# Kernel optimization log

Hardware: AMD Instinct MI355X
Metric: run time of the kernel (lower is better)

## Reference

```python
import jax, jax.numpy as jnp
import numpy as np

B, L, S, H, E = 4, 2048, 2048, 8, 64


def setup_inputs() -> dict:
    key = jax.random.key(0)
    kq, kk, kv, kt = jax.random.split(key, 4)
    queries = jax.random.normal(kq, (B, L, H, E), dtype=jnp.float32)
    keys = jax.random.normal(kk, (B, S, H, E), dtype=jnp.float32)
    values = jax.random.normal(kv, (B, S, H, E), dtype=jnp.float32)
    # de-stationarization log-scale factor, kept small so exp(tau) ~ O(1)
    tau = 0.1 * jax.random.normal(kt, (B, 1, 1, 1), dtype=jnp.float32)
    # causal mask: True above the diagonal (positions to be masked)
    attn_mask = jnp.triu(jnp.ones((L, S), dtype=bool), k=1)
    return {"queries": queries, "keys": keys, "values": values,
            "attn_mask": attn_mask, "tau": tau}


def reference(queries, keys, values, attn_mask, tau):
    # queries: [B,L,H,E], keys/values: [B,S,H,E], tau: [B,1,1,1], mask: [L,S]
    E_ = queries.shape[-1]
    scale = 1.0 / jnp.sqrt(jnp.asarray(E_, dtype=queries.dtype))
    # scores: [B,H,L,S], with tau-based de-stationarization rescale
    scores = jnp.einsum('blhe,bshe->bhls', queries, keys) * (scale * jnp.exp(tau))
    scores = jnp.where(attn_mask, -jnp.inf, scores)
    A = jax.nn.softmax(scores, axis=-1)  # dropout is identity at inference
    V = jnp.einsum('bhls,bshd->blhd', A, values)
    return V
```

## Files before the change

### kernel.cpp

```cpp
#include <hip/hip_runtime.h>
#include <hip/hip_bf16.h>
#include <math.h>

#define B_ 4
#define L_ 2048
#define H_ 8
#define E_ 64
#define HE 512

typedef short bf16x8 __attribute__((ext_vector_type(8)));
typedef float f32x4 __attribute__((ext_vector_type(4)));
typedef float f32x16 __attribute__((ext_vector_type(16)));
typedef unsigned short u16x4 __attribute__((ext_vector_type(4)));
typedef unsigned short u16x8 __attribute__((ext_vector_type(8)));

__device__ __forceinline__ unsigned short f2b(float f) {
  return __builtin_bit_cast(unsigned short, (__hip_bfloat16)f);
}
__device__ __forceinline__ unsigned cvtpk(float lo, float hi) {
  unsigned r;
  asm("v_cvt_pk_bf16_f32 %0, %1, %2" : "=v"(r) : "v"(lo), "v"(hi));
  return r;
}
__device__ __forceinline__ void pl32swap(unsigned &a, unsigned &b) {
  asm volatile("v_permlane32_swap_b32 %0, %1" : "+v"(a), "+v"(b));
}

__global__ __launch_bounds__(512, 1) void attn_fwd(
    const float* __restrict__ Q, const float* __restrict__ K,
    const float* __restrict__ V, const float* __restrict__ tau,
    float* __restrict__ O)
{
  const int f  = blockIdx.x + 16 * (blockIdx.y + 8 * blockIdx.z);
  const int u  = f >> 5, hb = f & 31;
  const int h  = hb & 7, b = hb >> 3;
  const int qt = (u < 8) ? u : 23 - u;

  const int tid  = threadIdx.x;
  const int wave = tid >> 6, lane = tid & 63;
  const int l31 = lane & 31, hi = lane >> 5;
  const int l7 = l31 & 7;
  const int half = wave >> 2, wv = wave & 3;

  __shared__ union {
    struct { unsigned short Kt[2][2][64 * 64];
             unsigned short Vt[2][2][64 * 64]; } kv;
    struct { float O[128][64]; float m[128]; float l[128]; } cmb;
  } sm;

  const float qscale = 0.125f * expf(tau[b]) * 1.44269504088896f;
  const int q0w = qt * 128 + wv * 32;
  const int myq = q0w + l31;
  const int dqd = 32 * wv + l31 - 64 * half;
  const bool skipw = (half == 1) && (wv < 2);

  const float* Qb = Q + (((size_t)b * L_ + myq) * H_ + h) * E_;
  bf16x8 qf[4];
  #pragma unroll
  for (int ks = 0; ks < 4; ++ks) {
    f32x4 a = *(const f32x4*)(Qb + ks * 16 + hi * 8);
    f32x4 c = *(const f32x4*)(Qb + ks * 16 + hi * 8 + 4);
    #pragma unroll
    for (int j = 0; j < 4; ++j) {
      qf[ks][j]     = (short)f2b(a[j] * qscale);
      qf[ks][4 + j] = (short)f2b(c[j] * qscale);
    }
  }

  float m_run = -INFINITY, l_run = 0.0f;
  f32x16 oacc[2];
  #pragma unroll
  for (int nd = 0; nd < 2; ++nd)
    #pragma unroll
    for (int r = 0; r < 16; ++r) oacc[nd][r] = 0.0f;

  const int hs = tid >> 8, st = tid & 255;
  const int krow = st >> 2, kcg = st & 3;
  const int vkv = (st & 15) * 4, vd = (st >> 4) * 4;
  const size_t bh = ((size_t)b * L_ * H_ + h) * E_;
  const float* Kp = K + bh + (size_t)(64 * hs + krow) * HE + kcg * 16;
  const float* Vp = V + bh + (size_t)(64 * hs + vkv) * HE + vd;
  const int kwo0 = krow * 64 + (((2 * kcg)     ^ (krow & 7)) << 3);
  const int kwo1 = krow * 64 + (((2 * kcg + 1) ^ (krow & 7)) << 3);

  const int nt = qt + 1;

  f32x4 kq[4], vq[4];
  #pragma unroll
  for (int i = 0; i < 4; ++i) kq[i] = *(const f32x4*)(Kp + 4 * i);
  #pragma unroll
  for (int i = 0; i < 4; ++i) vq[i] = *(const f32x4*)(Vp + (size_t)i * HE);
  {
    u16x8 w0, w1;
    #pragma unroll
    for (int j = 0; j < 4; ++j) {
      w0[j] = f2b(kq[0][j]); w0[4 + j] = f2b(kq[1][j]);
      w1[j] = f2b(kq[2][j]); w1[4 + j] = f2b(kq[3][j]);
    }
    *(u16x8*)(&sm.kv.Kt[hs][0][kwo0]) = w0;
    *(u16x8*)(&sm.kv.Kt[hs][0][kwo1]) = w1;
    #pragma unroll
    for (int jd = 0; jd < 4; ++jd) {
      const int row = vd + jd;
      u16x4 vw;
      #pragma unroll
      for (int i = 0; i < 4; ++i) vw[i] = f2b(vq[i][jd]);
      *(u16x4*)(&sm.kv.Vt[hs][0][row * 64 + (((vkv >> 3) ^ (row & 7)) << 3) + (vkv & 7)]) = vw;
    }
  }
  __syncthreads();
  int cur = 0;

  for (int t = 0; t < nt; ++t) {
    const bool havenext = (t + 1 < nt);
    if (havenext) {
      const float* Kn = Kp + (size_t)(t + 1) * 128 * HE;
      const float* Vn = Vp + (size_t)(t + 1) * 128 * HE;
      #pragma unroll
      for (int i = 0; i < 4; ++i) kq[i] = *(const f32x4*)(Kn + 4 * i);
      #pragma unroll
      for (int i = 0; i < 4; ++i) vq[i] = *(const f32x4*)(Vn + (size_t)i * HE);
    }

    if (!(skipw && t == nt - 1)) {
      const unsigned short* Kl = sm.kv.Kt[half][cur];
      const unsigned short* Vl = sm.kv.Vt[half][cur];

      f32x16 sacc[2];
      #pragma unroll
      for (int mt = 0; mt < 2; ++mt)
        #pragma unroll
        for (int r = 0; r < 16; ++r) sacc[mt][r] = 0.0f;
      __builtin_amdgcn_s_setprio(1);
      #pragma unroll
      for (int ks = 0; ks < 4; ++ks) {
        #pragma unroll
        for (int mt = 0; mt < 2; ++mt) {
          bf16x8 kf = *(const bf16x8*)(Kl + (32 * mt + l31) * 64 +
                                       (((2 * ks + hi) ^ l7) << 3));
          sacc[mt] = __builtin_amdgcn_mfma_f32_32x32x16_bf16(kf, qf[ks], sacc[mt], 0, 0, 0);
        }
      }
      __builtin_amdgcn_s_setprio(0);

      if (t == nt - 1) {
        #pragma unroll
        for (int mt = 0; mt < 2; ++mt)
          #pragma unroll
          for (int r = 0; r < 16; ++r) {
            const int kvl = 32 * mt + (r & 3) + 8 * (r >> 2) + 4 * hi;
            if (kvl > dqd) sacc[mt][r] = -3.0e38f;
          }
      }

      float p0 = sacc[0][0], p1 = sacc[0][1], p2 = sacc[0][2], p3 = sacc[0][3];
      #pragma unroll
      for (int mt = 0; mt < 2; ++mt)
        #pragma unroll
        for (int r = (mt == 0 ? 4 : 0); r < 16; r += 4) {
          p0 = fmaxf(p0, sacc[mt][r]);
          p1 = fmaxf(p1, sacc[mt][r + 1]);
          p2 = fmaxf(p2, sacc[mt][r + 2]);
          p3 = fmaxf(p3, sacc[mt][r + 3]);
        }
      float mx = fmaxf(fmaxf(p0, p1), fmaxf(p2, p3));
      mx = fmaxf(mx, __shfl_xor(mx, 32));

      if (!__all(mx - m_run <= 8.0f)) {
        const float mnew = fmaxf(m_run, mx);
        const float corr = exp2f(m_run - mnew);
        m_run = mnew;
        l_run *= corr;
        #pragma unroll
        for (int r = 0; r < 16; ++r) {
          const int qrow = (r & 3) + 8 * (r >> 2) + 4 * hi;
          const float cr = __shfl(corr, qrow);
          oacc[0][r] *= cr;
          oacc[1][r] *= cr;
        }
      }

      float s0 = 0.f, s1 = 0.f, s2 = 0.f, s3 = 0.f;
      #pragma unroll
      for (int mt = 0; mt < 2; ++mt)
        #pragma unroll
        for (int r = 0; r < 16; r += 4) {
          float e0 = exp2f(sacc[mt][r]     - m_run);
          float e1 = exp2f(sacc[mt][r + 1] - m_run);
          float e2 = exp2f(sacc[mt][r + 2] - m_run);
          float e3 = exp2f(sacc[mt][r + 3] - m_run);
          sacc[mt][r] = e0; sacc[mt][r + 1] = e1;
          sacc[mt][r + 2] = e2; sacc[mt][r + 3] = e3;
          s0 += e0; s1 += e1; s2 += e2; s3 += e3;
        }
      l_run += (s0 + s1) + (s2 + s3);

      unsigned pk[2][8];
      #pragma unroll
      for (int mt = 0; mt < 2; ++mt)
        #pragma unroll
        for (int i = 0; i < 8; ++i)
          pk[mt][i] = cvtpk(sacc[mt][2 * i], sacc[mt][2 * i + 1]);

      __builtin_amdgcn_s_setprio(1);
      #pragma unroll
      for (int ks = 0; ks < 4; ++ks) {
        const int c = ks & 1, mtx = ks >> 1;
        unsigned a  = pk[mtx][4 * c];
        unsigned y  = pk[mtx][4 * c + 2];
        unsigned a2 = pk[mtx][4 * c + 1];
        unsigned y2 = pk[mtx][4 * c + 3];
        pl32swap(a, y);
        pl32swap(a2, y2);
        union { unsigned w[4]; bf16x8 v; } pu;
        pu.w[0] = a; pu.w[1] = a2; pu.w[2] = y; pu.w[3] = y2;
        #pragma unroll
        for (int nd = 0; nd < 2; ++nd) {
          bf16x8 vf = *(const bf16x8*)(Vl + (32 * nd + l31) * 64 +
                                       (((2 * ks + hi) ^ l7) << 3));
          oacc[nd] = __builtin_amdgcn_mfma_f32_32x32x16_bf16(pu.v, vf, oacc[nd], 0, 0, 0);
        }
      }
      __builtin_amdgcn_s_setprio(0);
    }

    if (havenext) {
      const int nb = cur ^ 1;
      u16x8 w0, w1;
      #pragma unroll
      for (int j = 0; j < 4; ++j) {
        w0[j] = f2b(kq[0][j]); w0[4 + j] = f2b(kq[1][j]);
        w1[j] = f2b(kq[2][j]); w1[4 + j] = f2b(kq[3][j]);
      }
      *(u16x8*)(&sm.kv.Kt[hs][nb][kwo0]) = w0;
      *(u16x8*)(&sm.kv.Kt[hs][nb][kwo1]) = w1;
      #pragma unroll
      for (int jd = 0; jd < 4; ++jd) {
        const int row = vd + jd;
        u16x4 vw;
        #pragma unroll
        for (int i = 0; i < 4; ++i) vw[i] = f2b(vq[i][jd]);
        *(u16x4*)(&sm.kv.Vt[hs][nb][row * 64 + (((vkv >> 3) ^ (row & 7)) << 3) + (vkv & 7)]) = vw;
      }
      __syncthreads();
      cur = nb;
    }
  }

  l_run += __shfl_xor(l_run, 32);

  __syncthreads();
  if (half == 1) {
    #pragma unroll
    for (int r = 0; r < 16; ++r) {
      const int qrow = (r & 3) + 8 * (r >> 2) + 4 * hi;
      sm.cmb.O[32 * wv + qrow][l31]      = oacc[0][r];
      sm.cmb.O[32 * wv + qrow][32 + l31] = oacc[1][r];
    }
    if (hi == 0) { sm.cmb.m[32 * wv + l31] = m_run; sm.cmb.l[32 * wv + l31] = l_run; }
  }
  __syncthreads();
  if (half == 0) {
    const float m_b = sm.cmb.m[32 * wv + l31];
    const float l_b = sm.cmb.l[32 * wv + l31];
    const float mm = fmaxf(m_run, m_b);
    const float sa = exp2f(m_run - mm);
    const float sb = exp2f(m_b - mm);
    const float linv = 1.0f / (sa * l_run + sb * l_b);
    const float wa = sa * linv, wb = sb * linv;
    float* Ob = O + (((size_t)b * L_ + q0w) * H_ + h) * E_;
    #pragma unroll
    for (int r = 0; r < 16; ++r) {
      const int qrow = (r & 3) + 8 * (r >> 2) + 4 * hi;
      const float wa_r = __shfl(wa, qrow);
      const float wb_r = __shfl(wb, qrow);
      Ob[(size_t)qrow * HE + l31] =
          wa_r * oacc[0][r] + wb_r * sm.cmb.O[32 * wv + qrow][l31];
      Ob[(size_t)qrow * HE + 32 + l31] =
          wa_r * oacc[1][r] + wb_r * sm.cmb.O[32 * wv + qrow][32 + l31];
    }
  }
}

extern "C" void kernel_launch(void* const* d_in, const int* in_sizes, int n_in,
                              void* d_out, int out_size, void* d_ws, size_t ws_size,
                              hipStream_t stream) {
  (void)in_sizes; (void)n_in; (void)out_size; (void)d_ws; (void)ws_size;
  const float* Q   = (const float*)d_in[0];
  const float* K   = (const float*)d_in[1];
  const float* V   = (const float*)d_in[2];
  const float* tau = (const float*)d_in[4];
  float* O = (float*)d_out;
  dim3 grid(16, 8, 4), block(512);
  hipLaunchKernelGGL(attn_fwd, grid, block, 0, stream, Q, K, V, tau, O);
}
```

Before: 54.56 us.

## Precompute bf16 swizzled K/V tiles in a prep kernel, stream them in attention

Adds a prep kernel that converts K and V from fp32 to bf16 once, in the swizzled and transposed LDS layout, and writes them to workspace. The attention kernel then loads the ready-made tiles with plain 16-byte copies instead of re-reading fp32 and converting inside the loop. Causal tiles were re-read by many query tiles, so this halves global bytes per reload and removes conversion ALU work from the main loop. The cost is an extra kernel launch and a full fp32 read plus bf16 write of K/V.

```diff
diff --git a/kernel.cpp b/kernel.cpp
--- a/kernel.cpp
+++ b/kernel.cpp
@@ -26,9 +26,61 @@
   asm volatile("v_permlane32_swap_b32 %0, %1" : "+v"(a), "+v"(b));
 }
 
+__global__ __launch_bounds__(256) void prep(
+    const float* __restrict__ K, const float* __restrict__ V,
+    unsigned short* __restrict__ Kws, unsigned short* __restrict__ Vws)
+{
+  const int tile = blockIdx.x;
+  const int hb   = blockIdx.y;
+  const int h = hb & 7, b = hb >> 3;
+  const int st = threadIdx.x;
+
+  __shared__ unsigned short lK[64 * 64];
+  __shared__ unsigned short lV[64 * 64];
+
+  const int krow = st >> 2, kcg = st & 3;
+  const int vkv = (st & 15) * 4, vd = (st >> 4) * 4;
+  const size_t bh = ((size_t)b * L_ * H_ + h) * E_;
+  const float* Kp = K + bh + (size_t)(64 * tile + krow) * HE + kcg * 16;
+  const float* Vp = V + bh + (size_t)(64 * tile + vkv) * HE + vd;
+  const int kwo0 = krow * 64 + (((2 * kcg)     ^ (krow & 7)) << 3);
+  const int kwo1 = krow * 64 + (((2 * kcg + 1) ^ (krow & 7)) << 3);
+
+  f32x4 kq[4], vq[4];
+  #pragma unroll
+  for (int i = 0; i < 4; ++i) kq[i] = *(const f32x4*)(Kp + 4 * i);
+  #pragma unroll
+  for (int i = 0; i < 4; ++i) vq[i] = *(const f32x4*)(Vp + (size_t)i * HE);
+
+  u16x8 w0, w1;
+  #pragma unroll
+  for (int j = 0; j < 4; ++j) {
+    w0[j] = f2b(kq[0][j]); w0[4 + j] = f2b(kq[1][j]);
+    w1[j] = f2b(kq[2][j]); w1[4 + j] = f2b(kq[3][j]);
+  }
+  *(u16x8*)(&lK[kwo0]) = w0;
+  *(u16x8*)(&lK[kwo1]) = w1;
+  #pragma unroll
+  for (int jd = 0; jd < 4; ++jd) {
+    const int row = vd + jd;
+    u16x4 vw;
+    #pragma unroll
+    for (int i = 0; i < 4; ++i) vw[i] = f2b(vq[i][jd]);
+    *(u16x4*)(&lV[row * 64 + (((vkv >> 3) ^ (row & 7)) << 3) + (vkv & 7)]) = vw;
+  }
+  __syncthreads();
+
+  unsigned short* Kd = Kws + ((size_t)hb * 32 + tile) * 4096;
+  unsigned short* Vd = Vws + ((size_t)hb * 32 + tile) * 4096;
+  *(u16x8*)(Kd + st * 8)        = *(const u16x8*)(lK + st * 8);
+  *(u16x8*)(Kd + 2048 + st * 8) = *(const u16x8*)(lK + 2048 + st * 8);
+  *(u16x8*)(Vd + st * 8)        = *(const u16x8*)(lV + st * 8);
+  *(u16x8*)(Vd + 2048 + st * 8) = *(const u16x8*)(lV + 2048 + st * 8);
+}
+
 __global__ __launch_bounds__(512, 1) void attn_fwd(
-    const float* __restrict__ Q, const float* __restrict__ K,
-    const float* __restrict__ V, const float* __restrict__ tau,
+    const float* __restrict__ Q, const unsigned short* __restrict__ Kws,
+    const unsigned short* __restrict__ Vws, const float* __restrict__ tau,
     float* __restrict__ O)
 {
   const int f  = blockIdx.x + 16 * (blockIdx.y + 8 * blockIdx.z);
@@ -75,52 +127,35 @@
     for (int r = 0; r < 16; ++r) oacc[nd][r] = 0.0f;
 
   const int hs = tid >> 8, st = tid & 255;
-  const int krow = st >> 2, kcg = st & 3;
-  const int vkv = (st & 15) * 4, vd = (st >> 4) * 4;
-  const size_t bh = ((size_t)b * L_ * H_ + h) * E_;
-  const float* Kp = K + bh + (size_t)(64 * hs + krow) * HE + kcg * 16;
-  const float* Vp = V + bh + (size_t)(64 * hs + vkv) * HE + vd;
-  const int kwo0 = krow * 64 + (((2 * kcg)     ^ (krow & 7)) << 3);
-  const int kwo1 = krow * 64 + (((2 * kcg + 1) ^ (krow & 7)) << 3);
+  const unsigned short* Kb = Kws + (size_t)hb * 32 * 4096;
+  const unsigned short* Vb = Vws + (size_t)hb * 32 * 4096;
 
   const int nt = qt + 1;
 
-  f32x4 kq[4], vq[4];
-  #pragma unroll
-  for (int i = 0; i < 4; ++i) kq[i] = *(const f32x4*)(Kp + 4 * i);
-  #pragma unroll
-  for (int i = 0; i < 4; ++i) vq[i] = *(const f32x4*)(Vp + (size_t)i * HE);
-  {
-    u16x8 w0, w1;
-    #pragma unroll
-    for (int j = 0; j < 4; ++j) {
-      w0[j] = f2b(kq[0][j]); w0[4 + j] = f2b(kq[1][j]);
-      w1[j] = f2b(kq[2][j]); w1[4 + j] = f2b(kq[3][j]);
-    }
-    *(u16x8*)(&sm.kv.Kt[hs][0][kwo0]) = w0;
-    *(u16x8*)(&sm.kv.Kt[hs][0][kwo1]) = w1;
-    #pragma unroll
-    for (int jd = 0; jd < 4; ++jd) {
-      const int row = vd + jd;
-      u16x4 vw;
-      #pragma unroll
-      for (int i = 0; i < 4; ++i) vw[i] = f2b(vq[i][jd]);
-      *(u16x4*)(&sm.kv.Vt[hs][0][row * 64 + (((vkv >> 3) ^ (row & 7)) << 3) + (vkv & 7)]) = vw;
-    }
-  }
+  u16x8 kA, kB, vA, vB;
+  auto load_tile = [&](int t64) {
+    const unsigned short* Ks = Kb + (size_t)t64 * 4096;
+    const unsigned short* Vs = Vb + (size_t)t64 * 4096;
+    kA = *(const u16x8*)(Ks + st * 8);
+    kB = *(const u16x8*)(Ks + 2048 + st * 8);
+    vA = *(const u16x8*)(Vs + st * 8);
+    vB = *(const u16x8*)(Vs + 2048 + st * 8);
+  };
+  auto stage_write = [&](int nb) {
+    *(u16x8*)(&sm.kv.Kt[hs][nb][st * 8])        = kA;
+    *(u16x8*)(&sm.kv.Kt[hs][nb][2048 + st * 8]) = kB;
+    *(u16x8*)(&sm.kv.Vt[hs][nb][st * 8])        = vA;
+    *(u16x8*)(&sm.kv.Vt[hs][nb][2048 + st * 8]) = vB;
+  };
+
+  load_tile(hs);
+  stage_write(0);
   __syncthreads();
   int cur = 0;
 
   for (int t = 0; t < nt; ++t) {
     const bool havenext = (t + 1 < nt);
-    if (havenext) {
-      const float* Kn = Kp + (size_t)(t + 1) * 128 * HE;
-      const float* Vn = Vp + (size_t)(t + 1) * 128 * HE;
-      #pragma unroll
-      for (int i = 0; i < 4; ++i) kq[i] = *(const f32x4*)(Kn + 4 * i);
-      #pragma unroll
-      for (int i = 0; i < 4; ++i) vq[i] = *(const f32x4*)(Vn + (size_t)i * HE);
-    }
+    if (havenext) load_tile(2 * (t + 1) + hs);
 
     if (!(skipw && t == nt - 1)) {
       const unsigned short* Kl = sm.kv.Kt[half][cur];
@@ -225,25 +260,9 @@
     }
 
     if (havenext) {
-      const int nb = cur ^ 1;
-      u16x8 w0, w1;
-      #pragma unroll
-      for (int j = 0; j < 4; ++j) {
-        w0[j] = f2b(kq[0][j]); w0[4 + j] = f2b(kq[1][j]);
-        w1[j] = f2b(kq[2][j]); w1[4 + j] = f2b(kq[3][j]);
-      }
-      *(u16x8*)(&sm.kv.Kt[hs][nb][kwo0]) = w0;
-      *(u16x8*)(&sm.kv.Kt[hs][nb][kwo1]) = w1;
-      #pragma unroll
-      for (int jd = 0; jd < 4; ++jd) {
-        const int row = vd + jd;
-        u16x4 vw;
-        #pragma unroll
-        for (int i = 0; i < 4; ++i) vw[i] = f2b(vq[i][jd]);
-        *(u16x4*)(&sm.kv.Vt[hs][nb][row * 64 + (((vkv >> 3) ^ (row & 7)) << 3) + (vkv & 7)]) = vw;
-      }
+      stage_write(cur ^ 1);
       __syncthreads();
-      cur = nb;
+      cur ^= 1;
     }
   }
 
@@ -285,12 +304,17 @@
 extern "C" void kernel_launch(void* const* d_in, const int* in_sizes, int n_in,
                               void* d_out, int out_size, void* d_ws, size_t ws_size,
                               hipStream_t stream) {
-  (void)in_sizes; (void)n_in; (void)out_size; (void)d_ws; (void)ws_size;
+  (void)in_sizes; (void)n_in; (void)out_size; (void)ws_size;
   const float* Q   = (const float*)d_in[0];
   const float* K   = (const float*)d_in[1];
   const float* V   = (const float*)d_in[2];
   const float* tau = (const float*)d_in[4];
   float* O = (float*)d_out;
+
+  unsigned short* Kws = (unsigned short*)d_ws;
+  unsigned short* Vws = Kws + (size_t)32 * 32 * 4096;
+
+  hipLaunchKernelGGL(prep, dim3(32, 32), dim3(256), 0, stream, K, V, Kws, Vws);
   dim3 grid(16, 8, 4), block(512);
-  hipLaunchKernelGGL(attn_fwd, grid, block, 0, stream, Q, K, V, tau, O);
-}
+  hipLaunchKernelGGL(attn_fwd, grid, block, 0, stream, Q, Kws, Vws, tau, O);
+}
```

Result: slower. 58.77 us (+7.7%).
